# Optimization experiments

Measured on AMD Instinct MI355X. Metric: run time of the kernel, lower is better.

Reference implementation:

```python
import jax, jax.numpy as jnp
import numpy as np

DIM = 1024
N_HEADS = 16
HEAD_DIM = DIM // N_HEADS
HIDDEN = 4 * DIM
B, T = 4, 2048
EPS = 1e-5


def setup_inputs() -> dict:
    key = jax.random.key(0)
    ks = jax.random.split(key, 12)
    s = lambda fan_in: 1.0 / np.sqrt(fan_in)
    return {
        "x": jax.random.normal(ks[0], (B, T, DIM), jnp.float32),
        "ln1_g": jnp.ones((DIM,), jnp.float32),
        "ln1_b": jnp.zeros((DIM,), jnp.float32),
        "qkv_w": jax.random.normal(ks[1], (DIM, 3 * DIM), jnp.float32) * s(DIM),
        "qkv_b": jnp.zeros((3 * DIM,), jnp.float32),
        "proj_w": jax.random.normal(ks[2], (DIM, DIM), jnp.float32) * s(DIM),
        "proj_b": jnp.zeros((DIM,), jnp.float32),
        "ln2_g": jnp.ones((DIM,), jnp.float32),
        "ln2_b": jnp.zeros((DIM,), jnp.float32),
        "ff1_w": jax.random.normal(ks[3], (DIM, HIDDEN), jnp.float32) * s(DIM),
        "ff1_b": jnp.zeros((HIDDEN,), jnp.float32),
        "ff2_w": jax.random.normal(ks[4], (HIDDEN, DIM), jnp.float32) * s(HIDDEN),
        "ff2_b": jnp.zeros((DIM,), jnp.float32),
    }


def _layernorm(x, g, b):
    mu = jnp.mean(x, axis=-1, keepdims=True)
    var = jnp.mean(jnp.square(x - mu), axis=-1, keepdims=True)
    return (x - mu) * jax.lax.rsqrt(var + EPS) * g + b


def _attn(x, qkv_w, qkv_b, proj_w, proj_b):
    Bx, Tx, C = x.shape
    qkv = (x @ qkv_w + qkv_b).reshape(Bx, Tx, 3, N_HEADS, HEAD_DIM)
    q, k, v = (qkv[:, :, i].transpose(0, 2, 1, 3) for i in range(3))  # [B,H,T,hd]
    att = jnp.einsum('bhqd,bhkd->bhqk', q, k) / np.sqrt(HEAD_DIM)
    causal = jnp.tril(jnp.ones((Tx, Tx), bool))
    att = jnp.where(causal, att, -jnp.inf)
    att = jax.nn.softmax(att, axis=-1)
    out = jnp.einsum('bhqk,bhkd->bhqd', att, v).transpose(0, 2, 1, 3).reshape(Bx, Tx, C)
    return out @ proj_w + proj_b


def reference(x, ln1_g, ln1_b, qkv_w, qkv_b, proj_w, proj_b,
              ln2_g, ln2_b, ff1_w, ff1_b, ff2_w, ff2_b):
    x = x + _attn(_layernorm(x, ln1_g, ln1_b), qkv_w, qkv_b, proj_w, proj_b)
    h = _layernorm(x, ln2_g, ln2_b)
    h = jax.nn.gelu(h @ ff1_w + ff1_b, approximate=False) @ ff2_w + ff2_b
    return x + h
```

## Files before the change

kernel.cpp:

```cpp
#include <hip/hip_runtime.h>
#include <hip/hip_bf16.h>
#include <math.h>

#define DIM 1024
#define NHEADS 16
#define HD 64
#define TT 2048
#define BB 4
#define MTOK (BB*TT)
#define HID 4096

typedef __attribute__((ext_vector_type(8))) short bf16x8;
typedef __attribute__((ext_vector_type(4))) float f32x4;
typedef unsigned short u16;
typedef unsigned int u32;

__device__ inline u16 f2b(float f){
  __hip_bfloat16 h = __float2bfloat16(f);
  return __builtin_bit_cast(u16, h);
}

__device__ inline u32 cvtpk(float lo, float hi_){
  u32 r;
  asm("v_cvt_pk_bf16_f32 %0, %1, %2" : "=v"(r) : "v"(lo), "v"(hi_));
  return r;
}

__device__ inline void load_lds16(const void* g, void* l){
  __builtin_amdgcn_global_load_lds(
      (const __attribute__((address_space(1))) void*)g,
      (__attribute__((address_space(3))) void*)l,
      16, 0, 0);
}

__global__ __launch_bounds__(256) void wconv_t(const float* __restrict__ W,
                                               u16* __restrict__ Wt, int K, int N){
  __shared__ float tl[32][33];
  const int k0 = blockIdx.x*32, n0 = blockIdx.y*32;
  const int tx = threadIdx.x & 31, ty = threadIdx.x >> 5;
  #pragma unroll
  for (int r=0;r<32;r+=8)
    tl[ty+r][tx] = W[(size_t)(k0+ty+r)*N + (n0+tx)];
  __syncthreads();
  #pragma unroll
  for (int r=0;r<32;r+=8)
    Wt[(size_t)(n0+ty+r)*K + (k0+tx)] = f2b(tl[tx][ty+r]);
}

__global__ __launch_bounds__(256) void ln_fwd(const float* __restrict__ x,
                                              const float* __restrict__ g,
                                              const float* __restrict__ bta,
                                              u16* __restrict__ out){
  const int row = blockIdx.x, t = threadIdx.x;
  const float4 v = ((const float4*)(x + (size_t)row*DIM))[t];
  float s  = v.x+v.y+v.z+v.w;
  float s2 = v.x*v.x+v.y*v.y+v.z*v.z+v.w*v.w;
  #pragma unroll
  for (int m=1;m<64;m<<=1){ s += __shfl_xor(s,m); s2 += __shfl_xor(s2,m); }
  __shared__ float red[8];
  if ((t&63)==0){ red[t>>6]=s; red[4+(t>>6)]=s2; }
  __syncthreads();
  s  = red[0]+red[1]+red[2]+red[3];
  s2 = red[4]+red[5]+red[6]+red[7];
  const float mu = s*(1.0f/DIM);
  const float rstd = rsqrtf(s2*(1.0f/DIM) - mu*mu + 1e-5f);
  const float4 gv = ((const float4*)g)[t];
  const float4 bv = ((const float4*)bta)[t];
  ushort4 ov;
  ov.x = f2b((v.x-mu)*rstd*gv.x + bv.x);
  ov.y = f2b((v.y-mu)*rstd*gv.y + bv.y);
  ov.z = f2b((v.z-mu)*rstd*gv.z + bv.z);
  ov.w = f2b((v.w-mu)*rstd*gv.w + bv.w);
  ((ushort4*)out)[(size_t)row*(DIM/4) + t] = ov;
}

template<int EPI>
__global__ __launch_bounds__(512) void gemm_bt(
    const u16* __restrict__ A, const u16* __restrict__ Bt,
    const float* __restrict__ bias, const float* __restrict__ resid,
    float* __restrict__ outf, u16* __restrict__ outh,
    u16* __restrict__ qo, u16* __restrict__ ko, u16* __restrict__ vo,
    int M, int N, int K)
{
  __shared__ __align__(16) u16 smem[24576];
  u16* Ct = smem;
  const int t = threadIdx.x, wv = t>>6, ln = t&63;
  const int nbx = gridDim.x, nby = gridDim.y;
  const int bid = blockIdx.y*nbx + blockIdx.x;
  const int xcd = bid & 7, lid = bid >> 3;
  const int rpx = nby >> 3;
  const int m0 = (xcd*rpx + (lid % rpx)) * 128;
  const int n0 = (lid / rpx) * 128;
  const int wr = wv>>2, wc = wv&3;
  const int hi = ln>>4, lr = hi*4, lc = ln&15;
  f32x4 acc[4][2] = {};

  auto STAGE32 = [&](int buf, int kt){
    u16* As = smem + buf*8192;
    u16* Bs = smem + buf*8192 + 4096;
    const int row = t>>2, c = t&3;
    const int cs = c ^ ((row>>1)&3);
    load_lds16(A  + (size_t)(m0+row)*K + kt + cs*8, (char*)As + t*16);
    load_lds16(Bt + (size_t)(n0+row)*K + kt + cs*8, (char*)Bs + t*16);
  };
  auto RD32 = [&](const u16* base, int r)->bf16x8{
    return *(const bf16x8*)(base + r*32 + ((hi ^ ((r>>1)&3))<<3));
  };
  auto COMPUTE32 = [&](int buf){
    const u16* As = smem + buf*8192;
    const u16* Bs = smem + buf*8192 + 4096;
    bf16x8 af[4], bfr[2];
    #pragma unroll
    for (int mi=0;mi<4;mi++) af[mi] = RD32(As, wr*64 + mi*16 + lc);
    #pragma unroll
    for (int ni=0;ni<2;ni++) bfr[ni] = RD32(Bs, wc*32 + ni*16 + lc);
    __builtin_amdgcn_s_setprio(1);
    #pragma unroll
    for (int mi=0;mi<4;mi++)
      #pragma unroll
      for (int ni=0;ni<2;ni++)
        acc[mi][ni] = __builtin_amdgcn_mfma_f32_16x16x32_bf16(af[mi], bfr[ni], acc[mi][ni], 0,0,0);
    __builtin_amdgcn_s_setprio(0);
  };

  const int nk = K>>5;
  STAGE32(0, 0);
  STAGE32(1, 32);
  asm volatile("s_waitcnt vmcnt(2)" ::: "memory");
  __builtin_amdgcn_s_barrier();
  for (int tt=0; tt<nk; ++tt){
    if (tt+2 < nk) STAGE32((tt+2)%3, (tt+2)<<5);
    COMPUTE32(tt%3);
    if (tt+1 < nk){
      if (tt+2 < nk) asm volatile("s_waitcnt vmcnt(2)" ::: "memory");
      else           asm volatile("s_waitcnt vmcnt(0)" ::: "memory");
      __builtin_amdgcn_s_barrier();
    }
  }

  if constexpr (EPI==1 || EPI==3){
    #pragma unroll
    for (int ni=0;ni<2;ni++){
      const int gn = n0 + wc*32 + ni*16 + lc;
      const float bv = bias[gn];
      #pragma unroll
      for (int mi=0;mi<4;mi++){
        const int gmb = m0 + wr*64 + mi*16 + lr;
        f32x4 a = acc[mi][ni];
        #pragma unroll
        for (int i=0;i<4;i++){
          const size_t idx = (size_t)(gmb+i)*DIM + gn;
          outf[idx] = a[i] + bv + resid[idx];
        }
      }
    }
  } else {
    const int part = (EPI==0) ? (n0>>10) : 0;
    __syncthreads();
    #pragma unroll
    for (int ni=0;ni<2;ni++){
      const int gn = n0 + wc*32 + ni*16 + lc;
      const float bv = bias[gn];
      const int cl = wc*32 + ni*16 + lc;
      #pragma unroll
      for (int mi=0;mi<4;mi++){
        f32x4 a = acc[mi][ni];
        #pragma unroll
        for (int i=0;i<4;i++){
          const int rl = wr*64 + mi*16 + lr + i;
          float val = a[i] + bv;
          if constexpr (EPI==2){
            const float xx = val*val;
            const float w  = val * fmaf(xx, 0.10294322f, 2.30220781f);
            const float y  = exp2f(w);
            const float r_ = __builtin_amdgcn_rcpf(1.0f + y);
            val = val - val*r_;
          }
          int r = rl, c = cl;
          if (EPI==0 && part==2){ r = cl; c = rl; }
          const int chunk = c>>3;
          const int csw = (chunk&8) | ((chunk ^ (r&7)) & 7);
          Ct[(r<<7) + (csw<<3) + (c&7)] = f2b(val);
        }
      }
    }
    __syncthreads();
    const int cid = t & 7, rsub = t >> 3;
    const int bb = m0>>11, tok0b = m0&2047;
    const int h0 = (EPI==0) ? ((n0&1023)>>6) : 0;
    #pragma unroll
    for (int pass=0; pass<2; ++pass){
      const int rr = pass*64 + rsub;
      #pragma unroll
      for (int hh=0; hh<2; ++hh){
        const int chunk = hh*8 + cid;
        const int sw = (chunk&8) | ((chunk ^ (rr&7)) & 7);
        const bf16x8 vvv = *(const bf16x8*)&Ct[(rr<<7) + (sw<<3)];
        if constexpr (EPI==2){
          *(bf16x8*)&outh[(size_t)(m0+rr)*HID + n0 + chunk*8] = vvv;
        } else {
          if (part==2){
            const int head = h0 + (rr>>6), d = rr&63;
            *(bf16x8*)&vo[(((size_t)bb*NHEADS + head)*HD + d)*TT + tok0b + chunk*8] = vvv;
          } else {
            u16* dst = part ? ko : qo;
            const int head = h0 + hh;
            *(bf16x8*)&dst[(((size_t)bb*NHEADS + head)*TT + tok0b + rr)*HD + cid*8] = vvv;
          }
        }
      }
    }
  }
}

__global__ __launch_bounds__(512) void attn_fwd(
    const u16* __restrict__ qpt, const u16* __restrict__ kb, const u16* __restrict__ vtb,
    u16* __restrict__ o)
{
  __shared__ __align__(16) u16 Kd[3][64*64];
  __shared__ __align__(16) u16 Vd[3][64*64];
  const int t = threadIdx.x, wv = t>>6, ln = t&63;
  const int bid  = blockIdx.y*gridDim.x + blockIdx.x;
  const int orig = (bid&7)*64 + (bid>>3);
  const int bh   = orig>>3;
  const int qp   = orig&7;
  const int qbA  = qp, qbB = 15-qp;
  const size_t base = (size_t)bh*TT*HD;
  const int hi = ln>>4, lc = ln&15;
  const int ntA = 2*qbA + 2, ntB = 2*qbB + 2;
  const int qbaseA = qbA*128 + wv*16, qrowA = qbaseA + lc;
  const int qbaseB = qbB*128 + wv*16, qrowB = qbaseB + lc;

  const bf16x8 qfA0 = *(const bf16x8*)(qpt + base + (size_t)qrowA*HD + hi*8);
  const bf16x8 qfA1 = *(const bf16x8*)(qpt + base + (size_t)qrowA*HD + 32 + hi*8);
  const bf16x8 qfB0 = *(const bf16x8*)(qpt + base + (size_t)qrowB*HD + hi*8);
  const bf16x8 qfB1 = *(const bf16x8*)(qpt + base + (size_t)qrowB*HD + 32 + hi*8);
  f32x4 oaccA[4] = {}, oaccB[4] = {};
  f32x4 lsumA = {0.f,0.f,0.f,0.f}, lsumB = {0.f,0.f,0.f,0.f};
  float mrunA = -1e30f, mrunB = -1e30f;
  const float SCQ = 0.125f * 1.44269504f;
  bf16x8 ones;
  #pragma unroll
  for (int j=0;j<8;j++) ones[j] = (short)0x3F80;

  const int srow = t>>3;
  const int sch  = t&7;
  const int gch  = (sch ^ (srow&7))<<3;

  auto STAGE = [&](int nb, int kt){
    load_lds16(kb  + base + (size_t)(kt*64+srow)*HD + gch, &Kd[nb][srow*64 + sch*8]);
    load_lds16(vtb + base + (size_t)srow*TT + kt*64 + gch, &Vd[nb][srow*64 + sch*8]);
  };
  auto FRAG = [&](const u16* buf, int r, int ch)->bf16x8{
    return *(const bf16x8*)(buf + r*64 + ((ch ^ (r&7))<<3));
  };
  const int src0 = ((ln&16)<<1) + lc;
  const int src1 = src0 + 16;
  auto pick = [&](u32 w0, u32 w1, int src)->u32{
    const u32 a = (u32)__shfl((int)w0, src);
    const u32 b = (u32)__shfl((int)w1, src);
    return (hi<2) ? a : b;
  };

  auto strip_tile = [&](int kt, const u16* Kb, const u16* Vb,
                        const bf16x8& qf0, const bf16x8& qf1,
                        int qbase, int qrow,
                        f32x4* oacc, f32x4& lsum, float& mrun){
    if (kt*64 > qbase + 15) return;
    float sv[4][4];
    __builtin_amdgcn_s_setprio(1);
    #pragma unroll
    for (int cf=0;cf<4;cf++){
      const int r = cf*16 + lc;
      const bf16x8 kf0 = FRAG(Kb, r, hi);
      const bf16x8 kf1 = FRAG(Kb, r, hi+4);
      f32x4 z = {0.f,0.f,0.f,0.f};
      z = __builtin_amdgcn_mfma_f32_16x16x32_bf16(kf0, qf0, z, 0,0,0);
      z = __builtin_amdgcn_mfma_f32_16x16x32_bf16(kf1, qf1, z, 0,0,0);
      sv[cf][0]=z[0]; sv[cf][1]=z[1]; sv[cf][2]=z[2]; sv[cf][3]=z[3];
    }
    __builtin_amdgcn_s_setprio(0);
    float mx = -1e30f;
    if (kt*64 + 63 > qbase){
      #pragma unroll
      for (int cf=0;cf<4;cf++)
        #pragma unroll
        for (int i=0;i<4;i++){
          const int kvg = kt*64 + cf*16 + 4*hi + i;
          float s_ = sv[cf][i]*SCQ;
          s_ = (kvg > qrow) ? -1e30f : s_;
          sv[cf][i] = s_;
          mx = fmaxf(mx, s_);
        }
    } else {
      #pragma unroll
      for (int cf=0;cf<4;cf++)
        #pragma unroll
        for (int i=0;i<4;i++){
          const float s_ = sv[cf][i]*SCQ;
          sv[cf][i] = s_;
          mx = fmaxf(mx, s_);
        }
    }
    mx = fmaxf(mx, __shfl_xor(mx, 16));
    mx = fmaxf(mx, __shfl_xor(mx, 32));
    if (__any(mx > mrun + 11.0f)){
      const float mnew = fmaxf(mrun, mx);
      const float sc = exp2f(mrun - mnew);
      mrun = mnew;
      const float s0 = __shfl(sc, 4*hi+0);
      const float s1 = __shfl(sc, 4*hi+1);
      const float s2 = __shfl(sc, 4*hi+2);
      const float s3 = __shfl(sc, 4*hi+3);
      #pragma unroll
      for (int df=0;df<4;df++){
        oacc[df][0] *= s0; oacc[df][1] *= s1;
        oacc[df][2] *= s2; oacc[df][3] *= s3;
      }
      lsum[0] *= s0; lsum[1] *= s1; lsum[2] *= s2; lsum[3] *= s3;
    }
    u32 W[4][2];
    #pragma unroll
    for (int cf=0;cf<4;cf++){
      const float e0 = exp2f(sv[cf][0] - mrun);
      const float e1 = exp2f(sv[cf][1] - mrun);
      const float e2 = exp2f(sv[cf][2] - mrun);
      const float e3 = exp2f(sv[cf][3] - mrun);
      W[cf][0] = cvtpk(e0, e1);
      W[cf][1] = cvtpk(e2, e3);
    }
    uint4 uA, uB;
    uA.x = pick(W[0][0], W[1][0], src0);
    uA.y = pick(W[0][1], W[1][1], src0);
    uA.z = pick(W[0][0], W[1][0], src1);
    uA.w = pick(W[0][1], W[1][1], src1);
    uB.x = pick(W[2][0], W[3][0], src0);
    uB.y = pick(W[2][1], W[3][1], src0);
    uB.z = pick(W[2][0], W[3][0], src1);
    uB.w = pick(W[2][1], W[3][1], src1);
    const bf16x8 paA = __builtin_bit_cast(bf16x8, uA);
    const bf16x8 paB = __builtin_bit_cast(bf16x8, uB);
    __builtin_amdgcn_s_setprio(1);
    #pragma unroll
    for (int df=0;df<4;df++){
      const bf16x8 v0 = FRAG(Vb, df*16+lc, hi);
      const bf16x8 v1 = FRAG(Vb, df*16+lc, hi+4);
      oacc[df] = __builtin_amdgcn_mfma_f32_16x16x32_bf16(paA, v0, oacc[df], 0,0,0);
      oacc[df] = __builtin_amdgcn_mfma_f32_16x16x32_bf16(paB, v1, oacc[df], 0,0,0);
    }
    lsum = __builtin_amdgcn_mfma_f32_16x16x32_bf16(paA, ones, lsum, 0,0,0);
    lsum = __builtin_amdgcn_mfma_f32_16x16x32_bf16(paB, ones, lsum, 0,0,0);
    __builtin_amdgcn_s_setprio(0);
  };

  STAGE(0, 0);
  STAGE(1, 1);
  asm volatile("s_waitcnt vmcnt(2)" ::: "memory");
  __syncthreads();

  for (int kt=0; kt<ntB; kt++){
    if (kt+2 < ntB) STAGE((kt+2)%3, kt+2);
    const u16* Kb = Kd[kt%3];
    const u16* Vb = Vd[kt%3];
    strip_tile(kt, Kb, Vb, qfB0, qfB1, qbaseB, qrowB, oaccB, lsumB, mrunB);
    if (kt < ntA)
      strip_tile(kt, Kb, Vb, qfA0, qfA1, qbaseA, qrowA, oaccA, lsumA, mrunA);
    if (kt+1 < ntB){
      if (kt+2 < ntB) asm volatile("s_waitcnt vmcnt(2)" ::: "memory");
      else            asm volatile("s_waitcnt vmcnt(0)" ::: "memory");
      __syncthreads();
    }
  }

  const int b = bh>>4, h = bh&15;
  {
    const float inv[4] = {1.0f/lsumA[0], 1.0f/lsumA[1], 1.0f/lsumA[2], 1.0f/lsumA[3]};
    const int qg0 = qbaseA + 4*hi;
    #pragma unroll
    for (int i=0;i<4;i++){
      const size_t rowb = ((size_t)b*TT + (size_t)(qg0 + i))*DIM + h*HD;
      #pragma unroll
      for (int df=0;df<4;df++)
        o[rowb + df*16 + lc] = f2b(oaccA[df][i]*inv[i]);
    }
  }
  {
    const float inv[4] = {1.0f/lsumB[0], 1.0f/lsumB[1], 1.0f/lsumB[2], 1.0f/lsumB[3]};
    const int qg0 = qbaseB + 4*hi;
    #pragma unroll
    for (int i=0;i<4;i++){
      const size_t rowb = ((size_t)b*TT + (size_t)(qg0 + i))*DIM + h*HD;
      #pragma unroll
      for (int df=0;df<4;df++)
        o[rowb + df*16 + lc] = f2b(oaccB[df][i]*inv[i]);
    }
  }
}

extern "C" void kernel_launch(void* const* d_in, const int* in_sizes, int n_in,
                              void* d_out, int out_size, void* d_ws, size_t ws_size,
                              hipStream_t stream){
  (void)in_sizes; (void)n_in; (void)out_size; (void)ws_size;
  const float* x     = (const float*)d_in[0];
  const float* ln1g  = (const float*)d_in[1];
  const float* ln1b  = (const float*)d_in[2];
  const float* qkvw  = (const float*)d_in[3];
  const float* qkvb  = (const float*)d_in[4];
  const float* projw = (const float*)d_in[5];
  const float* projb = (const float*)d_in[6];
  const float* ln2g  = (const float*)d_in[7];
  const float* ln2b  = (const float*)d_in[8];
  const float* ff1w  = (const float*)d_in[9];
  const float* ff1b  = (const float*)d_in[10];
  const float* ff2w  = (const float*)d_in[11];
  const float* ff2b  = (const float*)d_in[12];
  float* out = (float*)d_out;

  char* ws = (char*)d_ws;
  size_t off = 0;
  auto alloc = [&](size_t n){ char* p = ws + off; off += (n + 255) & ~(size_t)255; return p; };
  u16* wqkvt  = (u16*)alloc((size_t)3072*1024*2);
  u16* wprojt = (u16*)alloc((size_t)1024*1024*2);
  u16* wff1t  = (u16*)alloc((size_t)4096*1024*2);
  u16* wff2t  = (u16*)alloc((size_t)1024*4096*2);
  u16* h1     = (u16*)alloc((size_t)MTOK*DIM*2);
  u16* qbuf   = (u16*)alloc((size_t)MTOK*DIM*2);
  u16* kbuf   = (u16*)alloc((size_t)MTOK*DIM*2);
  u16* vbuf   = (u16*)alloc((size_t)MTOK*DIM*2);
  u16* aout   = (u16*)alloc((size_t)MTOK*DIM*2);
  float* x2   = (float*)alloc((size_t)MTOK*DIM*4);
  u16* h2     = (u16*)alloc((size_t)MTOK*DIM*2);
  u16* act    = (u16*)alloc((size_t)MTOK*HID*2);

  wconv_t<<<dim3(1024/32, 3072/32), 256, 0, stream>>>(qkvw, wqkvt, 1024, 3072);
  wconv_t<<<dim3(1024/32, 1024/32), 256, 0, stream>>>(projw, wprojt, 1024, 1024);
  wconv_t<<<dim3(1024/32, 4096/32), 256, 0, stream>>>(ff1w, wff1t, 1024, 4096);
  wconv_t<<<dim3(4096/32, 1024/32), 256, 0, stream>>>(ff2w, wff2t, 4096, 1024);

  ln_fwd<<<MTOK, 256, 0, stream>>>(x, ln1g, ln1b, h1);

  gemm_bt<0><<<dim3(3072/128, MTOK/128), 512, 0, stream>>>(
      h1, wqkvt, qkvb, nullptr, nullptr, nullptr, qbuf, kbuf, vbuf, MTOK, 3072, 1024);

  attn_fwd<<<dim3(8, BB*NHEADS), 512, 0, stream>>>(qbuf, kbuf, vbuf, aout);

  gemm_bt<1><<<dim3(1024/128, MTOK/128), 512, 0, stream>>>(
      aout, wprojt, projb, x, x2, nullptr, nullptr, nullptr, nullptr, MTOK, 1024, 1024);

  ln_fwd<<<MTOK, 256, 0, stream>>>(x2, ln2g, ln2b, h2);

  gemm_bt<2><<<dim3(4096/128, MTOK/128), 512, 0, stream>>>(
      h2, wff1t, ff1b, nullptr, nullptr, act, nullptr, nullptr, nullptr, MTOK, HID, 1024);

  gemm_bt<3><<<dim3(1024/128, MTOK/128), 512, 0, stream>>>(
      act, wff2t, ff2b, x2, out, nullptr, nullptr, nullptr, nullptr, MTOK, DIM, HID);
}
```

Baseline: 409.1 us.

## Use 4-wave GEMM with 64x64 per-wave tiles and store residual stream in bf16

The GEMM drops from 8 waves to 4 per 128x128 tile. Each wave now computes a 64x64 sub-tile with 16 MFMAs per k-step, so fragments are reused more and LDS reads per MFMA go down. Staging is split into two loads per thread, and the waitcnt thresholds are adjusted to match. Separately, the post-attention residual x2 is now written as bf16 through the LDS-staged epilogue and read back as bf16 by LayerNorm2 and the final residual add. This cuts memory traffic, but the residual path loses precision, and halving the threads per block may reduce latency hiding.

After: 396.8 us, median of 3. 1.03x faster.

```diff
diff --git a/kernel.cpp b/kernel.cpp
--- a/kernel.cpp
+++ b/kernel.cpp
@@ -18,6 +18,10 @@
 __device__ inline u16 f2b(float f){
   __hip_bfloat16 h = __float2bfloat16(f);
   return __builtin_bit_cast(u16, h);
+}
+__device__ inline float b2f(u16 u){
+  __hip_bfloat16 h = __builtin_bit_cast(__hip_bfloat16, u);
+  return __bfloat162float(h);
 }
 
 __device__ inline u32 cvtpk(float lo, float hi_){
@@ -47,12 +51,20 @@
     Wt[(size_t)(n0+ty+r)*K + (k0+tx)] = f2b(tl[tx][ty+r]);
 }
 
-__global__ __launch_bounds__(256) void ln_fwd(const float* __restrict__ x,
+template<bool BF16IN>
+__global__ __launch_bounds__(256) void ln_fwd(const float* __restrict__ xf,
+                                              const u16* __restrict__ xh,
                                               const float* __restrict__ g,
                                               const float* __restrict__ bta,
                                               u16* __restrict__ out){
   const int row = blockIdx.x, t = threadIdx.x;
-  const float4 v = ((const float4*)(x + (size_t)row*DIM))[t];
+  float4 v;
+  if constexpr (BF16IN){
+    const ushort4 u = ((const ushort4*)(xh + (size_t)row*DIM))[t];
+    v.x = b2f(u.x); v.y = b2f(u.y); v.z = b2f(u.z); v.w = b2f(u.w);
+  } else {
+    v = ((const float4*)(xf + (size_t)row*DIM))[t];
+  }
   float s  = v.x+v.y+v.z+v.w;
   float s2 = v.x*v.x+v.y*v.y+v.z*v.z+v.w*v.w;
   #pragma unroll
@@ -75,9 +87,10 @@
 }
 
 template<int EPI>
-__global__ __launch_bounds__(512) void gemm_bt(
+__global__ __launch_bounds__(256) void gemm_bt(
     const u16* __restrict__ A, const u16* __restrict__ Bt,
     const float* __restrict__ bias, const float* __restrict__ resid,
+    const u16* __restrict__ residh,
     float* __restrict__ outf, u16* __restrict__ outh,
     u16* __restrict__ qo, u16* __restrict__ ko, u16* __restrict__ vo,
     int M, int N, int K)
@@ -91,17 +104,21 @@
   const int rpx = nby >> 3;
   const int m0 = (xcd*rpx + (lid % rpx)) * 128;
   const int n0 = (lid / rpx) * 128;
-  const int wr = wv>>2, wc = wv&3;
+  const int wr = wv>>1, wc = wv&1;
   const int hi = ln>>4, lr = hi*4, lc = ln&15;
-  f32x4 acc[4][2] = {};
+  f32x4 acc[4][4] = {};
 
   auto STAGE32 = [&](int buf, int kt){
     u16* As = smem + buf*8192;
     u16* Bs = smem + buf*8192 + 4096;
-    const int row = t>>2, c = t&3;
-    const int cs = c ^ ((row>>1)&3);
-    load_lds16(A  + (size_t)(m0+row)*K + kt + cs*8, (char*)As + t*16);
-    load_lds16(Bt + (size_t)(n0+row)*K + kt + cs*8, (char*)Bs + t*16);
+    #pragma unroll
+    for (int j=0;j<2;j++){
+      const int id = j*256 + t;
+      const int row = id>>2, c = id&3;
+      const int cs = c ^ ((row>>1)&3);
+      load_lds16(A  + (size_t)(m0+row)*K + kt + cs*8, (char*)As + id*16);
+      load_lds16(Bt + (size_t)(n0+row)*K + kt + cs*8, (char*)Bs + id*16);
+    }
   };
   auto RD32 = [&](const u16* base, int r)->bf16x8{
     return *(const bf16x8*)(base + r*32 + ((hi ^ ((r>>1)&3))<<3));
@@ -109,16 +126,16 @@
   auto COMPUTE32 = [&](int buf){
     const u16* As = smem + buf*8192;
     const u16* Bs = smem + buf*8192 + 4096;
-    bf16x8 af[4], bfr[2];
+    bf16x8 af[4], bfr[4];
     #pragma unroll
     for (int mi=0;mi<4;mi++) af[mi] = RD32(As, wr*64 + mi*16 + lc);
     #pragma unroll
-    for (int ni=0;ni<2;ni++) bfr[ni] = RD32(Bs, wc*32 + ni*16 + lc);
+    for (int ni=0;ni<4;ni++) bfr[ni] = RD32(Bs, wc*64 + ni*16 + lc);
     __builtin_amdgcn_s_setprio(1);
     #pragma unroll
     for (int mi=0;mi<4;mi++)
       #pragma unroll
-      for (int ni=0;ni<2;ni++)
+      for (int ni=0;ni<4;ni++)
         acc[mi][ni] = __builtin_amdgcn_mfma_f32_16x16x32_bf16(af[mi], bfr[ni], acc[mi][ni], 0,0,0);
     __builtin_amdgcn_s_setprio(0);
   };
@@ -126,22 +143,22 @@
   const int nk = K>>5;
   STAGE32(0, 0);
   STAGE32(1, 32);
-  asm volatile("s_waitcnt vmcnt(2)" ::: "memory");
+  asm volatile("s_waitcnt vmcnt(4)" ::: "memory");
   __builtin_amdgcn_s_barrier();
   for (int tt=0; tt<nk; ++tt){
     if (tt+2 < nk) STAGE32((tt+2)%3, (tt+2)<<5);
     COMPUTE32(tt%3);
     if (tt+1 < nk){
-      if (tt+2 < nk) asm volatile("s_waitcnt vmcnt(2)" ::: "memory");
+      if (tt+2 < nk) asm volatile("s_waitcnt vmcnt(4)" ::: "memory");
       else           asm volatile("s_waitcnt vmcnt(0)" ::: "memory");
       __builtin_amdgcn_s_barrier();
     }
   }
 
-  if constexpr (EPI==1 || EPI==3){
-    #pragma unroll
-    for (int ni=0;ni<2;ni++){
-      const int gn = n0 + wc*32 + ni*16 + lc;
+  if constexpr (EPI==3){
+    #pragma unroll
+    for (int ni=0;ni<4;ni++){
+      const int gn = n0 + wc*64 + ni*16 + lc;
       const float bv = bias[gn];
       #pragma unroll
       for (int mi=0;mi<4;mi++){
@@ -150,7 +167,7 @@
         #pragma unroll
         for (int i=0;i<4;i++){
           const size_t idx = (size_t)(gmb+i)*DIM + gn;
-          outf[idx] = a[i] + bv + resid[idx];
+          outf[idx] = a[i] + bv + b2f(residh[idx]);
         }
       }
     }
@@ -158,10 +175,10 @@
     const int part = (EPI==0) ? (n0>>10) : 0;
     __syncthreads();
     #pragma unroll
-    for (int ni=0;ni<2;ni++){
-      const int gn = n0 + wc*32 + ni*16 + lc;
+    for (int ni=0;ni<4;ni++){
+      const int gn = n0 + wc*64 + ni*16 + lc;
       const float bv = bias[gn];
-      const int cl = wc*32 + ni*16 + lc;
+      const int cl = wc*64 + ni*16 + lc;
       #pragma unroll
       for (int mi=0;mi<4;mi++){
         f32x4 a = acc[mi][ni];
@@ -175,6 +192,8 @@
             const float y  = exp2f(w);
             const float r_ = __builtin_amdgcn_rcpf(1.0f + y);
             val = val - val*r_;
+          } else if constexpr (EPI==1){
+            val += resid[(size_t)(m0+rl)*DIM + gn];
           }
           int r = rl, c = cl;
           if (EPI==0 && part==2){ r = cl; c = rl; }
@@ -189,8 +208,8 @@
     const int bb = m0>>11, tok0b = m0&2047;
     const int h0 = (EPI==0) ? ((n0&1023)>>6) : 0;
     #pragma unroll
-    for (int pass=0; pass<2; ++pass){
-      const int rr = pass*64 + rsub;
+    for (int pass=0; pass<4; ++pass){
+      const int rr = pass*32 + rsub;
       #pragma unroll
       for (int hh=0; hh<2; ++hh){
         const int chunk = hh*8 + cid;
@@ -198,6 +217,8 @@
         const bf16x8 vvv = *(const bf16x8*)&Ct[(rr<<7) + (sw<<3)];
         if constexpr (EPI==2){
           *(bf16x8*)&outh[(size_t)(m0+rr)*HID + n0 + chunk*8] = vvv;
+        } else if constexpr (EPI==1){
+          *(bf16x8*)&outh[(size_t)(m0+rr)*DIM + n0 + chunk*8] = vvv;
         } else {
           if (part==2){
             const int head = h0 + (rr>>6), d = rr&63;
@@ -428,7 +449,7 @@
   u16* kbuf   = (u16*)alloc((size_t)MTOK*DIM*2);
   u16* vbuf   = (u16*)alloc((size_t)MTOK*DIM*2);
   u16* aout   = (u16*)alloc((size_t)MTOK*DIM*2);
-  float* x2   = (float*)alloc((size_t)MTOK*DIM*4);
+  u16* x2h    = (u16*)alloc((size_t)MTOK*DIM*2);
   u16* h2     = (u16*)alloc((size_t)MTOK*DIM*2);
   u16* act    = (u16*)alloc((size_t)MTOK*HID*2);
 
@@ -437,21 +458,21 @@
   wconv_t<<<dim3(1024/32, 4096/32), 256, 0, stream>>>(ff1w, wff1t, 1024, 4096);
   wconv_t<<<dim3(4096/32, 1024/32), 256, 0, stream>>>(ff2w, wff2t, 4096, 1024);
 
-  ln_fwd<<<MTOK, 256, 0, stream>>>(x, ln1g, ln1b, h1);
-
-  gemm_bt<0><<<dim3(3072/128, MTOK/128), 512, 0, stream>>>(
-      h1, wqkvt, qkvb, nullptr, nullptr, nullptr, qbuf, kbuf, vbuf, MTOK, 3072, 1024);
+  ln_fwd<false><<<MTOK, 256, 0, stream>>>(x, nullptr, ln1g, ln1b, h1);
+
+  gemm_bt<0><<<dim3(3072/128, MTOK/128), 256, 0, stream>>>(
+      h1, wqkvt, qkvb, nullptr, nullptr, nullptr, nullptr, qbuf, kbuf, vbuf, MTOK, 3072, 1024);
 
   attn_fwd<<<dim3(8, BB*NHEADS), 512, 0, stream>>>(qbuf, kbuf, vbuf, aout);
 
-  gemm_bt<1><<<dim3(1024/128, MTOK/128), 512, 0, stream>>>(
-      aout, wprojt, projb, x, x2, nullptr, nullptr, nullptr, nullptr, MTOK, 1024, 1024);
-
-  ln_fwd<<<MTOK, 256, 0, stream>>>(x2, ln2g, ln2b, h2);
-
-  gemm_bt<2><<<dim3(4096/128, MTOK/128), 512, 0, stream>>>(
-      h2, wff1t, ff1b, nullptr, nullptr, act, nullptr, nullptr, nullptr, MTOK, HID, 1024);
-
-  gemm_bt<3><<<dim3(1024/128, MTOK/128), 512, 0, stream>>>(
-      act, wff2t, ff2b, x2, out, nullptr, nullptr, nullptr, nullptr, MTOK, DIM, HID);
-}
+  gemm_bt<1><<<dim3(1024/128, MTOK/128), 256, 0, stream>>>(
+      aout, wprojt, projb, x, nullptr, nullptr, x2h, nullptr, nullptr, nullptr, MTOK, 1024, 1024);
+
+  ln_fwd<true><<<MTOK, 256, 0, stream>>>(nullptr, x2h, ln2g, ln2b, h2);
+
+  gemm_bt<2><<<dim3(4096/128, MTOK/128), 256, 0, stream>>>(
+      h2, wff1t, ff1b, nullptr, nullptr, nullptr, act, nullptr, nullptr, nullptr, MTOK, HID, 1024);
+
+  gemm_bt<3><<<dim3(1024/128, MTOK/128), 256, 0, stream>>>(
+      act, wff2t, ff2b, nullptr, x2h, out, nullptr, nullptr, nullptr, nullptr, MTOK, DIM, HID);
+}
```
